# Kernel tuning notes

Measured on AMD Instinct MI355X. Metric: run time of the kernel, lower is better.

Reference implementation:

```python
import jax, jax.numpy as jnp
import numpy as np
import math

B, S, H = 2, 4096, 512
NUM_HEADS = 8
HEAD_DIM = H // NUM_HEADS
RECENCY_DECAY = 0.9


def setup_inputs() -> dict:
    key = jax.random.key(0)
    k1, k2, k3 = jax.random.split(key, 3)
    scale = 1.0 / math.sqrt(H)
    x = jax.random.normal(k1, (B, S, H), dtype=jnp.float32)
    w_qkv = jax.random.normal(k2, (3 * H, H), dtype=jnp.float32) * scale
    w_out = jax.random.normal(k3, (H, H), dtype=jnp.float32) * scale
    b_out = jnp.zeros((H,), dtype=jnp.float32)
    return {"x": x, "w_qkv": w_qkv, "w_out": w_out, "b_out": b_out}


def reference(x, w_qkv, w_out, b_out):
    batch, seq_len, hidden = x.shape
    nh, hd = NUM_HEADS, HEAD_DIM
    # qkv projection (no bias): torch Linear computes x @ W.T
    qkv = jnp.einsum('bsh,oh->bso', x, w_qkv)
    qkv = qkv.reshape(batch, seq_len, 3, nh, hd)
    q, k, v = jnp.transpose(qkv, (2, 0, 3, 1, 4))  # each [B, nh, S, hd]
    attn = jnp.einsum('bhqd,bhkd->bhqk', q, k) / math.sqrt(hd)
    # recency bias: positions[i, j] = j - i; bias = (j-i)*log(decay) for j<=i else 0
    pos = jnp.arange(seq_len)[None, :] - jnp.arange(seq_len)[:, None]
    bias = jnp.where(pos <= 0, pos.astype(jnp.float32) * math.log(RECENCY_DECAY),
                     jnp.zeros((), dtype=jnp.float32))
    attn = jax.nn.softmax(attn + bias[None, None, :, :], axis=-1)
    out = jnp.einsum('bhqk,bhkd->bqhd', attn, v).reshape(batch, seq_len, hidden)
    return jnp.einsum('bsh,oh->bso', out, w_out) + b_out
```

## Files before the change

kernel.cpp:

```cpp
#include <hip/hip_runtime.h>
#include <hip/hip_bf16.h>
#include <stdint.h>

#define B_   2
#define S_   4096
#define H_   512
#define NH_  8
#define HD_  64
#define M_   (B_*S_)
#define LOG2D (-0.15200309344504997f)
#define SC2   (0.18033688011112042f)

#define NFULL        6
#define NCHUNK       8

typedef __attribute__((ext_vector_type(8))) short bf16x8_t;
typedef __attribute__((ext_vector_type(4))) float f32x4_t;

__device__ __forceinline__ void gl_lds16(const __hip_bfloat16* g, __hip_bfloat16* l) {
  __builtin_amdgcn_global_load_lds(
      (__attribute__((address_space(1))) void*)(g),
      (__attribute__((address_space(3))) void*)(l),
      16, 0, 0);
}

__global__ __launch_bounds__(256)
void cast3_kernel(const float* __restrict__ x, const float* __restrict__ wq,
                  const float* __restrict__ wo,
                  __hip_bfloat16* __restrict__ xb, __hip_bfloat16* __restrict__ wqb,
                  __hip_bfloat16* __restrict__ wob) {
  const int N0 = M_ * H_;
  const int N1 = 3 * H_ * H_;
  int i4 = (blockIdx.x * blockDim.x + threadIdx.x) * 4;
  const float* src; __hip_bfloat16* dst; int off;
  if (i4 < N0)           { src = x;  dst = xb;  off = i4; }
  else if (i4 < N0 + N1) { src = wq; dst = wqb; off = i4 - N0; }
  else                   { src = wo; dst = wob; off = i4 - N0 - N1; }
  float4 v = *(const float4*)(src + off);
  ushort4 o;
  __hip_bfloat16 h;
  h = __float2bfloat16(v.x); o.x = *(unsigned short*)&h;
  h = __float2bfloat16(v.y); o.y = *(unsigned short*)&h;
  h = __float2bfloat16(v.z); o.z = *(unsigned short*)&h;
  h = __float2bfloat16(v.w); o.w = *(unsigned short*)&h;
  *(ushort4*)((unsigned short*)dst + off) = o;
}

template<int EPI>
__global__ __launch_bounds__(256)
void gemm_bt(const __hip_bfloat16* __restrict__ A,
             const __hip_bfloat16* __restrict__ Bw,
             int K,
             __hip_bfloat16* __restrict__ qb,
             __hip_bfloat16* __restrict__ kb,
             __hip_bfloat16* __restrict__ vtb,
             float* __restrict__ outp,
             const float* __restrict__ bias) {
  __shared__ alignas(16) __hip_bfloat16 sA[128*32];
  __shared__ alignas(16) __hip_bfloat16 sB[128*32];
  const int tid  = threadIdx.x;
  const int wave = tid >> 6, lane = tid & 63;
  const int quad = lane >> 4, l15 = lane & 15;
  const int wr = (wave >> 1) * 64, wc = (wave & 1) * 64;
  const int m0 = blockIdx.y * 128, n0 = blockIdx.x * 128;

  f32x4_t acc[4][4] = {};

  for (int kt = 0; kt < K; kt += 32) {
    __syncthreads();
    #pragma unroll
    for (int cc = 0; cc < 2; cc++) {
      int c   = wave * 2 + cc;
      int row = c * 16 + (lane >> 2);
      int col = (lane & 3) * 8;
      gl_lds16(A  + (size_t)(m0 + row) * K + kt + col, sA + c * 512);
      gl_lds16(Bw + (size_t)(n0 + row) * K + kt + col, sB + c * 512);
    }
    __syncthreads();
    bf16x8_t af[4], bfr[4];
    #pragma unroll
    for (int x = 0; x < 4; x++)
      af[x] = *(const bf16x8_t*)(sA + (wr + x*16 + l15)*32 + quad*8);
    #pragma unroll
    for (int y = 0; y < 4; y++)
      bfr[y] = *(const bf16x8_t*)(sB + (wc + y*16 + l15)*32 + quad*8);
    #pragma unroll
    for (int x = 0; x < 4; x++)
      #pragma unroll
      for (int y = 0; y < 4; y++)
        acc[x][y] = __builtin_amdgcn_mfma_f32_16x16x32_bf16(af[x], bfr[y], acc[x][y], 0, 0, 0);
  }

  #pragma unroll
  for (int x = 0; x < 4; x++) {
    #pragma unroll
    for (int y = 0; y < 4; y++) {
      #pragma unroll
      for (int r = 0; r < 4; r++) {
        int gr = m0 + wr + x*16 + quad*4 + r;
        int gc = n0 + wc + y*16 + l15;
        float v = acc[x][y][r];
        if (EPI == 0) {
          int bb = gr >> 12, s = gr & 4095;
          int t  = gc >> 9,  rem = gc & 511;
          int h  = rem >> 6, d = rem & 63;
          __hip_bfloat16 hv = __float2bfloat16(v);
          int bh = bb * NH_ + h;
          if (t == 0)      qb [((size_t)bh * S_ + s) * HD_ + d] = hv;
          else if (t == 1) kb [((size_t)bh * S_ + s) * HD_ + d] = hv;
          else             vtb[((size_t)bh * HD_ + d) * S_ + s] = hv;
        } else {
          outp[(size_t)gr * H_ + gc] = v + bias[gc];
        }
      }
    }
  }
}

__global__ __launch_bounds__(256)
void attn_kernel(const __hip_bfloat16* __restrict__ qb,
                 const __hip_bfloat16* __restrict__ kb,
                 const __hip_bfloat16* __restrict__ vtb,
                 __hip_bfloat16* __restrict__ ob,
                 float* __restrict__ pO,
                 float* __restrict__ pl) {
  __shared__ alignas(16) __hip_bfloat16 sK[128*64];
  __shared__ alignas(16) __hip_bfloat16 sV[64*128];
  __shared__ alignas(16) __hip_bfloat16 sP[4][16*128];

  const int tid  = threadIdx.x;
  const int wave = tid >> 6, lane = tid & 63;
  const int quad = lane >> 4, l15 = lane & 15;
  const int w  = blockIdx.x;
  const int bh = blockIdx.y;

  int qt, jt0;
  bool direct;
  if (w < 58) { qt = 6 + w;     jt0 = 0;            direct = true;  }
  else        { int t = w - 58; qt = t >> 3; jt0 = (t & 7) * 4; direct = false; }
  const int q0 = qt * 64;

  const int qr = q0 + wave * 16 + l15;
  const __hip_bfloat16* qrow = qb + ((size_t)bh * S_ + qr) * HD_;
  bf16x8_t aQ0 = *(const bf16x8_t*)(qrow + quad * 8);
  bf16x8_t aQ1 = *(const bf16x8_t*)(qrow + 32 + quad * 8);

  f32x4_t accO[4] = {};
  float l_r[4];
  float negM2[4];
  const int row_i = q0 + wave * 16 + quad * 4;
  #pragma unroll
  for (int r = 0; r < 4; r++) {
    l_r[r] = 0.f;
    negM2[r] = -(17.312340f + 0.15200309344504997f * (float)(row_i + r));
  }

  const int subK  = lane >> 3;
  const int plogK = (lane & 7) ^ subK;
  const int subV  = lane >> 4;

  for (int it = 0; it < 4; ++it) {
    const int j0 = (jt0 + it) * 128;
    __syncthreads();
    #pragma unroll
    for (int cc = 0; cc < 4; cc++) {
      int c = wave * 4 + cc;
      int rK = c * 8 + subK;
      gl_lds16(kb + ((size_t)bh * S_ + j0 + rK) * HD_ + plogK * 8, sK + c * 512);
      int rV = c * 4 + subV;
      int plogV = (lane & 15) ^ (rV & 15);
      gl_lds16(vtb + ((size_t)bh * HD_ + rV) * S_ + j0 + plogV * 8, sV + c * 512);
    }
    __syncthreads();

    f32x4_t sfr[8];
    #pragma unroll
    for (int ni = 0; ni < 8; ni++) {
      int row = ni * 16 + l15;
      f32x4_t a = {};
      bf16x8_t b0 = *(const bf16x8_t*)(sK + row * 64 + ((quad       ^ (row & 7)) << 3));
      bf16x8_t b1 = *(const bf16x8_t*)(sK + row * 64 + (((quad + 4) ^ (row & 7)) << 3));
      a = __builtin_amdgcn_mfma_f32_16x16x32_bf16(aQ0, b0, a, 0, 0, 0);
      a = __builtin_amdgcn_mfma_f32_16x16x32_bf16(aQ1, b1, a, 0, 0, 0);
      sfr[ni] = a;
    }

    __hip_bfloat16* sPw = &sP[wave][0];
    #pragma unroll
    for (int r = 0; r < 4; r++) {
      const float d0 = (float)(j0 + l15 - (row_i + r));
      const int   row = quad * 4 + r;
      float psum = 0.f;
      #pragma unroll
      for (int ni = 0; ni < 8; ni++) {
        float dij = d0 + (float)(ni * 16);
        float arg = fmaf(fminf(dij, 0.f), LOG2D, fmaf(sfr[ni][r], SC2, negM2[r]));
        float p = __builtin_amdgcn_exp2f(arg);
        psum += p;
        int col = ni * 16 + l15;
        int phys = ((col >> 3) ^ (row & 15)) << 3;
        sPw[row * 128 + phys + (col & 7)] = __float2bfloat16(p);
      }
      l_r[r] += psum;
    }
    __builtin_amdgcn_sched_barrier(0);
    __builtin_amdgcn_s_waitcnt(0);
    __builtin_amdgcn_sched_barrier(0);

    #pragma unroll
    for (int kk = 0; kk < 4; kk++) {
      int pos = kk * 4 + quad;
      bf16x8_t aP = *(const bf16x8_t*)(sPw + l15 * 128 + ((pos ^ l15) << 3));
      #pragma unroll
      for (int nd = 0; nd < 4; nd++) {
        int row = nd * 16 + l15;
        bf16x8_t bV = *(const bf16x8_t*)(sV + row * 128 + ((pos ^ (row & 15)) << 3));
        accO[nd] = __builtin_amdgcn_mfma_f32_16x16x32_bf16(aP, bV, accO[nd], 0, 0, 0);
      }
    }
  }

  if (direct) {
    #pragma unroll
    for (int r = 0; r < 4; r++) {
      float l = l_r[r];
      #pragma unroll
      for (int msk = 1; msk < 16; msk <<= 1) l += __shfl_xor(l, msk, 64);
      l_r[r] = 1.0f / l;
    }
    const int b = bh >> 3, h = bh & 7;
    #pragma unroll
    for (int nd = 0; nd < 4; nd++)
      #pragma unroll
      for (int r = 0; r < 4; r++) {
        int srow = q0 + wave * 16 + quad * 4 + r;
        int col  = h * HD_ + nd * 16 + l15;
        ob[((size_t)b * S_ + srow) * H_ + col] = __float2bfloat16(accO[nd][r] * l_r[r]);
      }
  } else {
    #pragma unroll
    for (int r = 0; r < 4; r++) {
      float l = l_r[r];
      #pragma unroll
      for (int msk = 1; msk < 16; msk <<= 1) l += __shfl_xor(l, msk, 64);
      l_r[r] = l;
    }
    size_t base = ((size_t)bh * NFULL + qt) * NCHUNK + (size_t)(jt0 >> 2);
    float* po = pO + base * 4096;
    #pragma unroll
    for (int nd = 0; nd < 4; nd++)
      #pragma unroll
      for (int r = 0; r < 4; r++)
        po[(wave*16 + quad*4 + r) * 64 + nd*16 + l15] = accO[nd][r];
    if (l15 == 0) {
      #pragma unroll
      for (int r = 0; r < 4; r++)
        pl[base * 64 + wave*16 + quad*4 + r] = l_r[r];
    }
  }
}

__global__ __launch_bounds__(256)
void combine_kernel(const float* __restrict__ pO,
                    const float* __restrict__ pl,
                    __hip_bfloat16* __restrict__ ob) {
  const int f  = blockIdx.x;
  const int bh = blockIdx.y;
  const int tid = threadIdx.x;
  const int rr = tid >> 2, cg = (tid & 3) * 16;
  const size_t base0 = ((size_t)bh * NFULL + f) * NCHUNK;

  float L = 0.f;
  #pragma unroll
  for (int c = 0; c < NCHUNK; c++) L += pl[(base0 + c) * 64 + rr];
  const float inv = 1.0f / L;

  float o[16];
  #pragma unroll
  for (int k = 0; k < 16; k++) o[k] = 0.f;
  #pragma unroll
  for (int c = 0; c < NCHUNK; c++) {
    const float4* src = (const float4*)(pO + (base0 + c) * 4096 + rr * 64 + cg);
    #pragma unroll
    for (int k4 = 0; k4 < 4; k4++) {
      float4 v = src[k4];
      o[k4*4+0] += v.x; o[k4*4+1] += v.y;
      o[k4*4+2] += v.z; o[k4*4+3] += v.w;
    }
  }
  const int b = bh >> 3, h = bh & 7, s = f * 64 + rr;
  __hip_bfloat16* dst = ob + ((size_t)b * S_ + s) * H_ + h * HD_ + cg;
  #pragma unroll
  for (int k = 0; k < 16; k++) dst[k] = __float2bfloat16(o[k] * inv);
}

extern "C" void kernel_launch(void* const* d_in, const int* in_sizes, int n_in,
                              void* d_out, int out_size, void* d_ws, size_t ws_size,
                              hipStream_t stream) {
  const float* x     = (const float*)d_in[0];
  const float* w_qkv = (const float*)d_in[1];
  const float* w_out = (const float*)d_in[2];
  const float* b_out = (const float*)d_in[3];
  float* out = (float*)d_out;

  char* ws = (char*)d_ws;
  __hip_bfloat16* xb  = (__hip_bfloat16*)(ws);
  __hip_bfloat16* wqb = (__hip_bfloat16*)(ws + (8u  << 20));
  __hip_bfloat16* wob = (__hip_bfloat16*)(ws + (10u << 20));
  __hip_bfloat16* qb  = (__hip_bfloat16*)(ws + (11u << 20));
  __hip_bfloat16* kb  = (__hip_bfloat16*)(ws + (19u << 20));
  __hip_bfloat16* vtb = (__hip_bfloat16*)(ws + (27u << 20));
  float*          pO  = (float*)(ws + (36u << 20));
  float*          pl  = (float*)(ws + (49u << 20));
  __hip_bfloat16* ab  = xb;

  cast3_kernel<<<dim3(5120), dim3(256), 0, stream>>>(x, w_qkv, w_out, xb, wqb, wob);
  gemm_bt<0><<<dim3(12, 64), dim3(256), 0, stream>>>(xb, wqb, H_, qb, kb, vtb, nullptr, nullptr);
  attn_kernel<<<dim3(58 + NFULL * NCHUNK, B_ * NH_), dim3(256), 0, stream>>>(qb, kb, vtb, ab, pO, pl);
  combine_kernel<<<dim3(NFULL, B_ * NH_), dim3(256), 0, stream>>>(pO, pl, ab);
  gemm_bt<1><<<dim3(4, 64), dim3(256), 0, stream>>>(ab, wob, H_, nullptr, nullptr, nullptr, out, b_out);
}
```

Measured before the change: 158.8 us.

## Double-buffer K/V tiles in LDS and specialize softmax bias per tile mode

Adds a second LDS buffer for the K and V tiles. The next tile's global-to-LDS loads are issued right after the per-iteration barrier, so they overlap the QK MFMAs, softmax and PV work on the current tile. The wait before the PV stage now covers only LDS operations, relying on the next barrier's fence to complete the outstanding vector-memory loads. The softmax exponent is also split into three cases: tiles fully below the diagonal use a precomputed per-column bias, tiles fully above skip the bias, and only diagonal tiles keep the fminf path. The cost is more LDS per block, which may reduce occupancy.

```diff
diff --git a/kernel.cpp b/kernel.cpp
--- a/kernel.cpp
+++ b/kernel.cpp
@@ -117,6 +117,25 @@
   }
 }
 
+__device__ __forceinline__ void stage_kv(const __hip_bfloat16* __restrict__ kb,
+                                         const __hip_bfloat16* __restrict__ vtb,
+                                         int bh, int j0,
+                                         __hip_bfloat16* dK, __hip_bfloat16* dV,
+                                         int wave, int lane) {
+  const int subK  = lane >> 3;
+  const int plogK = (lane & 7) ^ subK;
+  const int subV  = lane >> 4;
+  #pragma unroll
+  for (int cc = 0; cc < 4; cc++) {
+    int c = wave * 4 + cc;
+    int rK = c * 8 + subK;
+    gl_lds16(kb + ((size_t)bh * S_ + j0 + rK) * HD_ + plogK * 8, dK + c * 512);
+    int rV = c * 4 + subV;
+    int plogV = (lane & 15) ^ (rV & 15);
+    gl_lds16(vtb + ((size_t)bh * HD_ + rV) * S_ + j0 + plogV * 8, dV + c * 512);
+  }
+}
+
 __global__ __launch_bounds__(256)
 void attn_kernel(const __hip_bfloat16* __restrict__ qb,
                  const __hip_bfloat16* __restrict__ kb,
@@ -124,8 +143,8 @@
                  __hip_bfloat16* __restrict__ ob,
                  float* __restrict__ pO,
                  float* __restrict__ pl) {
-  __shared__ alignas(16) __hip_bfloat16 sK[128*64];
-  __shared__ alignas(16) __hip_bfloat16 sV[64*128];
+  __shared__ alignas(16) __hip_bfloat16 sK[2][128*64];
+  __shared__ alignas(16) __hip_bfloat16 sV[2][64*128];
   __shared__ alignas(16) __hip_bfloat16 sP[4][16*128];
 
   const int tid  = threadIdx.x;
@@ -152,59 +171,87 @@
   #pragma unroll
   for (int r = 0; r < 4; r++) {
     l_r[r] = 0.f;
-    negM2[r] = -(17.312340f + 0.15200309344504997f * (float)(row_i + r));
-  }
-
-  const int subK  = lane >> 3;
-  const int plogK = (lane & 7) ^ subK;
-  const int subV  = lane >> 4;
+    negM2[r] = -(17.312340f - LOG2D * (float)(row_i + r));
+  }
+
+  stage_kv(kb, vtb, bh, jt0 * 128, &sK[0][0], &sV[0][0], wave, lane);
 
   for (int it = 0; it < 4; ++it) {
     const int j0 = (jt0 + it) * 128;
     __syncthreads();
-    #pragma unroll
-    for (int cc = 0; cc < 4; cc++) {
-      int c = wave * 4 + cc;
-      int rK = c * 8 + subK;
-      gl_lds16(kb + ((size_t)bh * S_ + j0 + rK) * HD_ + plogK * 8, sK + c * 512);
-      int rV = c * 4 + subV;
-      int plogV = (lane & 15) ^ (rV & 15);
-      gl_lds16(vtb + ((size_t)bh * HD_ + rV) * S_ + j0 + plogV * 8, sV + c * 512);
-    }
-    __syncthreads();
+    if (it < 3)
+      stage_kv(kb, vtb, bh, (jt0 + it + 1) * 128,
+               &sK[(it + 1) & 1][0], &sV[(it + 1) & 1][0], wave, lane);
+
+    const __hip_bfloat16* cK = &sK[it & 1][0];
+    const __hip_bfloat16* cV = &sV[it & 1][0];
 
     f32x4_t sfr[8];
     #pragma unroll
     for (int ni = 0; ni < 8; ni++) {
       int row = ni * 16 + l15;
       f32x4_t a = {};
-      bf16x8_t b0 = *(const bf16x8_t*)(sK + row * 64 + ((quad       ^ (row & 7)) << 3));
-      bf16x8_t b1 = *(const bf16x8_t*)(sK + row * 64 + (((quad + 4) ^ (row & 7)) << 3));
+      bf16x8_t b0 = *(const bf16x8_t*)(cK + row * 64 + ((quad       ^ (row & 7)) << 3));
+      bf16x8_t b1 = *(const bf16x8_t*)(cK + row * 64 + (((quad + 4) ^ (row & 7)) << 3));
       a = __builtin_amdgcn_mfma_f32_16x16x32_bf16(aQ0, b0, a, 0, 0, 0);
       a = __builtin_amdgcn_mfma_f32_16x16x32_bf16(aQ1, b1, a, 0, 0, 0);
       sfr[ni] = a;
     }
 
     __hip_bfloat16* sPw = &sP[wave][0];
-    #pragma unroll
-    for (int r = 0; r < 4; r++) {
-      const float d0 = (float)(j0 + l15 - (row_i + r));
-      const int   row = quad * 4 + r;
-      float psum = 0.f;
-      #pragma unroll
-      for (int ni = 0; ni < 8; ni++) {
-        float dij = d0 + (float)(ni * 16);
-        float arg = fmaf(fminf(dij, 0.f), LOG2D, fmaf(sfr[ni][r], SC2, negM2[r]));
-        float p = __builtin_amdgcn_exp2f(arg);
-        psum += p;
-        int col = ni * 16 + l15;
-        int phys = ((col >> 3) ^ (row & 15)) << 3;
-        sPw[row * 128 + phys + (col & 7)] = __float2bfloat16(p);
-      }
-      l_r[r] += psum;
+    const int mode = (j0 + 128 <= q0) ? 0 : ((j0 >= q0 + 64) ? 1 : 2);
+    if (mode == 0) {
+      float cj[8];
+      #pragma unroll
+      for (int ni = 0; ni < 8; ni++)
+        cj[ni] = fmaf((float)(j0 + ni * 16 + l15), LOG2D, -17.312340f);
+      #pragma unroll
+      for (int r = 0; r < 4; r++) {
+        const int row = quad * 4 + r;
+        float psum = 0.f;
+        #pragma unroll
+        for (int ni = 0; ni < 8; ni++) {
+          float p = __builtin_amdgcn_exp2f(fmaf(sfr[ni][r], SC2, cj[ni]));
+          psum += p;
+          int col = ni * 16 + l15;
+          sPw[row * 128 + (((col >> 3) ^ (row & 15)) << 3) + (col & 7)] = __float2bfloat16(p);
+        }
+        l_r[r] += psum;
+      }
+    } else if (mode == 1) {
+      #pragma unroll
+      for (int r = 0; r < 4; r++) {
+        const int row = quad * 4 + r;
+        float psum = 0.f;
+        #pragma unroll
+        for (int ni = 0; ni < 8; ni++) {
+          float p = __builtin_amdgcn_exp2f(fmaf(sfr[ni][r], SC2, negM2[r]));
+          psum += p;
+          int col = ni * 16 + l15;
+          sPw[row * 128 + (((col >> 3) ^ (row & 15)) << 3) + (col & 7)] = __float2bfloat16(p);
+        }
+        l_r[r] += psum;
+      }
+    } else {
+      #pragma unroll
+      for (int r = 0; r < 4; r++) {
+        const float d0 = (float)(j0 + l15 - (row_i + r));
+        const int row = quad * 4 + r;
+        float psum = 0.f;
+        #pragma unroll
+        for (int ni = 0; ni < 8; ni++) {
+          float dij = d0 + (float)(ni * 16);
+          float arg = fmaf(fminf(dij, 0.f), LOG2D, fmaf(sfr[ni][r], SC2, negM2[r]));
+          float p = __builtin_amdgcn_exp2f(arg);
+          psum += p;
+          int col = ni * 16 + l15;
+          sPw[row * 128 + (((col >> 3) ^ (row & 15)) << 3) + (col & 7)] = __float2bfloat16(p);
+        }
+        l_r[r] += psum;
+      }
     }
     __builtin_amdgcn_sched_barrier(0);
-    __builtin_amdgcn_s_waitcnt(0);
+    __builtin_amdgcn_s_waitcnt(0xC07F);
     __builtin_amdgcn_sched_barrier(0);
 
     #pragma unroll
@@ -214,7 +261,7 @@
       #pragma unroll
       for (int nd = 0; nd < 4; nd++) {
         int row = nd * 16 + l15;
-        bf16x8_t bV = *(const bf16x8_t*)(sV + row * 128 + ((pos ^ (row & 15)) << 3));
+        bf16x8_t bV = *(const bf16x8_t*)(cV + row * 128 + ((pos ^ (row & 15)) << 3));
         accO[nd] = __builtin_amdgcn_mfma_f32_16x16x32_bf16(aP, bV, accO[nd], 0, 0, 0);
       }
     }
```

After: 162.3 us. 1.02x slower.
